# Performance work log

Measured on AMD Instinct MI355X. Metric: run time of the kernel, lower is better.

Reference implementation:

```python
import jax, jax.numpy as jnp
import numpy as np

NUM_EMBEDDINGS = 512
EMBEDDING_DIM = 128
COMMITMENT = 0.25
DECAY = 0.99
EPS = 1e-05


def setup_inputs() -> dict:
    key = jax.random.key(0)
    k1, k2 = jax.random.split(key)
    z = jax.random.normal(k1, (32, EMBEDDING_DIM, 64, 64), dtype=jnp.float32)
    embedding = jax.random.normal(k2, (EMBEDDING_DIM, NUM_EMBEDDINGS), dtype=jnp.float32)
    cluster_size = jnp.zeros((NUM_EMBEDDINGS,), dtype=jnp.float32)
    embed_avg = embedding  # buffer initialized as a clone of embedding
    return {"z": z, "embedding": embedding, "cluster_size": cluster_size, "embed_avg": embed_avg}


def reference(z, embedding, cluster_size, embed_avg):
    sg = jax.lax.stop_gradient
    D, K = embedding.shape
    B, C, H, W = z.shape
    z_perm = jnp.transpose(z, (0, 2, 3, 1))          # [B,H,W,D]
    flat_z = z_perm.reshape(-1, D)                    # [N,D]

    distances = ((flat_z ** 2).sum(1, keepdims=True)
                 - 2.0 * (flat_z @ embedding)
                 + (embedding ** 2).sum(0)[None, :])  # [N,K]
    idx = jnp.argmin(distances, axis=1)               # [N]

    # gather codes (equivalent to one-hot @ embedding.T, without materializing one-hot)
    quantized = jnp.take(embedding.T, idx, axis=0).reshape(z_perm.shape)  # [B,H,W,D]
    quantized = jnp.transpose(quantized, (0, 3, 1, 2))                    # [B,D,H,W]

    # EMA codebook update (training branch)
    enc_sum = jax.ops.segment_sum(jnp.ones_like(idx, dtype=flat_z.dtype), idx, num_segments=K)  # [K]
    embed_sum = jax.ops.segment_sum(flat_z, idx, num_segments=K).T                              # [D,K]
    new_cluster_size = cluster_size * DECAY + (1.0 - DECAY) * enc_sum
    new_embed_avg = embed_avg * DECAY + (1.0 - DECAY) * embed_sum
    n = jnp.maximum(new_cluster_size.sum(), 1e-05)
    cs = (new_cluster_size + EPS) / (n + K * EPS) * n
    new_embedding = new_embed_avg / cs[None, :]

    e_latent_loss = jnp.mean((sg(quantized) - z) ** 2)
    q_latent_loss = jnp.mean((quantized - sg(z)) ** 2)
    loss = q_latent_loss + COMMITMENT * e_latent_loss

    quantized_out = z + sg(quantized - z)             # straight-through
    encoding_indices = idx.reshape(B, H, W)
    return (quantized_out, loss, encoding_indices, new_embedding, new_cluster_size, new_embed_avg)
```

## Files before the change

### kernel.cpp

```cpp
#include <hip/hip_runtime.h>
#include <hip/hip_bf16.h>
#include <float.h>

typedef _Float16 f16;
typedef __attribute__((ext_vector_type(8))) _Float16 half8;
typedef __attribute__((ext_vector_type(4))) float floatx4;

#define DIM   128
#define HW    4096
#define NPOS  131072
#define K     512
#define ZSTRIDE_B 524288

#define Q_OFF     0
#define LOSS_OFF  16777216
#define IDX_OFF   16777217
#define NEMB_OFF  16908289
#define NCS_OFF   16973825
#define NEA_OFF   16974337

#define WS_E2    0
#define WS_ENC   512
#define WS_ESUM  1024
#define WS_EHI   1024
#define WS_ELO   33792
#define WS_LOSS  66560
#define WS_NN    66561

#define XST 136

__global__ __launch_bounds__(256) void k_prep(const float* __restrict__ emb,
                                              f16* __restrict__ ehiP,
                                              f16* __restrict__ eloP,
                                              float* __restrict__ e2) {
    int lin = blockIdx.x * 256 + threadIdx.x;
    int d = lin >> 9, k = lin & 511;
    float v = emb[lin];
    unsafeAtomicAdd(&e2[k], v * v);
    f16 h = (f16)v;
    f16 l = (f16)(v - (float)h);
    int g = k >> 4, r = k & 15;
    int dc = d >> 5, w = d & 31, quad = w >> 3, j = w & 7;
    int idx = (g * 4 + dc) * 512 + quad * 128 + r * 8 + j;
    ehiP[idx] = h;
    eloP[idx] = l;
}

__global__ __launch_bounds__(256, 2) void k_assign(const float* __restrict__ z,
                                                   const f16* __restrict__ ehiP,
                                                   const f16* __restrict__ eloP,
                                                   const float* __restrict__ e2,
                                                   float* __restrict__ out,
                                                   float* __restrict__ lossAcc) {
    __shared__ f16 xs_h[64 * XST];
    __shared__ f16 xs_l[64 * XST];
    __shared__ float wbD[256];
    __shared__ int   wbI[256];
    __shared__ int   bidx[64];
    __shared__ float wred[4];

    const int tid  = threadIdx.x;
    const int lane = tid & 63;
    const int wv   = tid >> 6;
    const int n0   = blockIdx.x * 64;
    const int b    = n0 >> 12;
    const int hw0  = n0 & 4095;
    const float* zb = z + b * ZSTRIDE_B + hw0;
    const int l15  = lane & 15;
    const int quad = lane >> 4;

    float sv0[16], sv1[16];
    #pragma unroll
    for (int it = 0; it < 16; ++it) {
        int lin = tid + it * 256;
        int i  = lin & 63;
        int dp = lin >> 6;
        sv0[it] = zb[(2 * dp) * HW + i];
        sv1[it] = zb[(2 * dp + 1) * HW + i];
    }
    #pragma unroll
    for (int it = 0; it < 16; ++it) {
        int lin = tid + it * 256;
        int i  = lin & 63;
        int dp = lin >> 6;
        float v0 = sv0[it], v1 = sv1[it];
        f16 h0 = (f16)v0; f16 l0 = (f16)(v0 - (float)h0);
        f16 h1 = (f16)v1; f16 l1 = (f16)(v1 - (float)h1);
        union { f16 h[2]; unsigned int u; } ph, pl;
        ph.h[0] = h0; ph.h[1] = h1;
        pl.h[0] = l0; pl.h[1] = l1;
        *(unsigned int*)&xs_h[i * XST + 2 * dp] = ph.u;
        *(unsigned int*)&xs_l[i * XST + 2 * dp] = pl.u;
    }
    __syncthreads();

    float bestD[4][4];
    int   bestI[4][4];
    #pragma unroll
    for (int t = 0; t < 4; ++t)
        #pragma unroll
        for (int r = 0; r < 4; ++r) { bestD[t][r] = FLT_MAX; bestI[t][r] = 0x7fffffff; }

    const half8* gh = (const half8*)ehiP;
    const half8* gl = (const half8*)eloP;

    for (int cc = 0; cc < 4; ++cc) {
        floatx4 acc[4][2];
        #pragma unroll
        for (int t = 0; t < 4; ++t)
            #pragma unroll
            for (int nt = 0; nt < 2; ++nt) acc[t][nt] = (floatx4){0.f, 0.f, 0.f, 0.f};

        for (int dc = 0; dc < 4; ++dc) {
            half8 ah[4], al[4];
            #pragma unroll
            for (int t = 0; t < 4; ++t) {
                int off = (t * 16 + l15) * XST + dc * 32 + quad * 8;
                ah[t] = *(const half8*)&xs_h[off];
                al[t] = *(const half8*)&xs_l[off];
            }
            #pragma unroll
            for (int nt = 0; nt < 2; ++nt) {
                int g  = cc * 8 + wv * 2 + nt;
                int bi = (g * 4 + dc) * 64 + lane;
                half8 bh = gh[bi];
                half8 bl = gl[bi];
                #pragma unroll
                for (int t = 0; t < 4; ++t) {
                    acc[t][nt] = __builtin_amdgcn_mfma_f32_16x16x32_f16(ah[t], bh, acc[t][nt], 0, 0, 0);
                    acc[t][nt] = __builtin_amdgcn_mfma_f32_16x16x32_f16(al[t], bh, acc[t][nt], 0, 0, 0);
                    acc[t][nt] = __builtin_amdgcn_mfma_f32_16x16x32_f16(ah[t], bl, acc[t][nt], 0, 0, 0);
                }
            }
        }
        #pragma unroll
        for (int nt = 0; nt < 2; ++nt) {
            int c = cc * 128 + wv * 32 + nt * 16 + l15;
            float ee = e2[c];
            #pragma unroll
            for (int t = 0; t < 4; ++t)
                #pragma unroll
                for (int r = 0; r < 4; ++r) {
                    float s = fmaf(-2.f, acc[t][nt][r], ee);
                    if (s < bestD[t][r]) { bestD[t][r] = s; bestI[t][r] = c; }
                }
        }
    }

    #pragma unroll
    for (int mask = 1; mask <= 8; mask <<= 1) {
        #pragma unroll
        for (int t = 0; t < 4; ++t)
            #pragma unroll
            for (int r = 0; r < 4; ++r) {
                float od = __shfl_xor(bestD[t][r], mask, 64);
                int   oi = __shfl_xor(bestI[t][r], mask, 64);
                if (od < bestD[t][r] || (od == bestD[t][r] && oi < bestI[t][r])) {
                    bestD[t][r] = od; bestI[t][r] = oi;
                }
            }
    }
    if (l15 == 0) {
        #pragma unroll
        for (int t = 0; t < 4; ++t)
            #pragma unroll
            for (int r = 0; r < 4; ++r) {
                int m = t * 16 + quad * 4 + r;
                wbD[wv * 64 + m] = bestD[t][r];
                wbI[wv * 64 + m] = bestI[t][r];
            }
    }
    __syncthreads();
    if (tid < 64) {
        float bd = wbD[tid]; int bi = wbI[tid];
        #pragma unroll
        for (int w = 1; w < 4; ++w) {
            float od = wbD[w * 64 + tid]; int oi = wbI[w * 64 + tid];
            if (od < bd || (od == bd && oi < bi)) { bd = od; bi = oi; }
        }
        bidx[tid] = bi;
        out[IDX_OFF + n0 + tid] = (float)bi;
    }
    __syncthreads();

    float* qb = out + Q_OFF + b * ZSTRIDE_B + hw0;
    float lsum = 0.f;
    #pragma unroll
    for (int it = 0; it < 4; ++it) {
        int o = wv * 4 + it;
        int c = bidx[lane];
        int g = c >> 4, r = c & 15;
        int base = (g * 4 + (o >> 2)) * 512 + (o & 3) * 128 + r * 8;
        half8 hh = *(const half8*)&ehiP[base];
        half8 ll = *(const half8*)&eloP[base];
        half8 zh = *(const half8*)&xs_h[lane * XST + o * 8];
        half8 zl = *(const half8*)&xs_l[lane * XST + o * 8];
        #pragma unroll
        for (int jj = 0; jj < 8; ++jj) {
            float q  = (float)hh[jj] + (float)ll[jj];
            float zz = (float)zh[jj] + (float)zl[jj];
            qb[(o * 8 + jj) * HW + lane] = q;
            float df = q - zz;
            lsum = fmaf(df, df, lsum);
        }
    }
    #pragma unroll
    for (int m = 32; m >= 1; m >>= 1) lsum += __shfl_xor(lsum, m, 64);
    if (lane == 0) wred[wv] = lsum;
    __syncthreads();
    if (tid == 0) unsafeAtomicAdd(lossAcc, wred[0] + wred[1] + wred[2] + wred[3]);
}

#define DC 8
__global__ __launch_bounds__(256) void k_ema2(const float* __restrict__ z,
                                              const float* __restrict__ out,
                                              float* __restrict__ enc,
                                              float* __restrict__ esum) {
    __shared__ float acc[DC][K];
    __shared__ float cnt[K];

    const int tid = threadIdx.x;
    const int half   = blockIdx.x & 1;
    const int dchunk = (blockIdx.x >> 1) & 15;
    const int b      = blockIdx.x >> 5;
    const int d0 = dchunk * DC;
    const bool doCnt = (dchunk == 0);

    for (int i = tid; i < DC * K; i += 256) ((float*)acc)[i] = 0.f;
    if (doCnt) for (int i = tid; i < K; i += 256) cnt[i] = 0.f;
    __syncthreads();

    const float* zb  = z + b * ZSTRIDE_B;
    const float* idp = out + IDX_OFF + b * HW;

    const int p0 = half * 2048;
    for (int t = p0; t < p0 + 2048; t += 1024) {
        const int p = t + 4 * tid;
        float4 iv = *(const float4*)(idp + p);
        int k0 = (int)iv.x;
        int k1 = (int)iv.y;
        int k2 = (int)iv.z;
        int k3 = (int)iv.w;
        if (doCnt) {
            atomicAdd(&cnt[k0], 1.f); atomicAdd(&cnt[k1], 1.f);
            atomicAdd(&cnt[k2], 1.f); atomicAdd(&cnt[k3], 1.f);
        }
        #pragma unroll
        for (int d = 0; d < DC; ++d) {
            float4 zv = *(const float4*)(zb + (d0 + d) * HW + p);
            atomicAdd(&acc[d][k0], zv.x);
            atomicAdd(&acc[d][k1], zv.y);
            atomicAdd(&acc[d][k2], zv.z);
            atomicAdd(&acc[d][k3], zv.w);
        }
    }
    __syncthreads();

    const int rot = (blockIdx.x & 31) << 6;
    for (int i = tid; i < DC * K; i += 256) {
        int j = (i + rot) & (DC * K - 1);
        int d = j >> 9, k = j & 511;
        unsafeAtomicAdd(&esum[(d0 + d) * K + k], acc[d][k]);
    }
    if (doCnt) for (int i = tid; i < K; i += 256) unsafeAtomicAdd(&enc[i], cnt[i]);
}

__global__ __launch_bounds__(512) void k_final(const float* __restrict__ enc,
                                               const float* __restrict__ cs_in,
                                               const float* __restrict__ lossAcc,
                                               float* __restrict__ out,
                                               float* __restrict__ nnOut) {
    __shared__ float red[512];
    int k = threadIdx.x;
    float ncs = fmaf(cs_in[k], 0.99f, 0.01f * enc[k]);
    red[k] = ncs;
    out[NCS_OFF + k] = ncs;
    __syncthreads();
    for (int s = 256; s > 0; s >>= 1) {
        if (k < s) red[k] += red[k + s];
        __syncthreads();
    }
    if (k == 0) {
        nnOut[0] = fmaxf(red[0], 1e-5f);
        out[LOSS_OFF] = lossAcc[0] * 1.25f / 16777216.0f;
    }
}

__global__ __launch_bounds__(512) void k_final2(const float* __restrict__ esum,
                                                const float* __restrict__ eavg_in,
                                                const float* __restrict__ nnIn,
                                                float* __restrict__ out) {
    int d = blockIdx.x;
    int k = threadIdx.x;
    float nn = nnIn[0];
    float ncs = out[NCS_OFF + k];
    float cs = (ncs + 1e-5f) / (nn + (float)K * 1e-5f) * nn;
    float ea = fmaf(eavg_in[d * K + k], 0.99f, 0.01f * esum[d * K + k]);
    out[NEA_OFF + d * K + k] = ea;
    out[NEMB_OFF + d * K + k] = ea / cs;
}

extern "C" void kernel_launch(void* const* d_in, const int* in_sizes, int n_in,
                              void* d_out, int out_size, void* d_ws, size_t ws_size,
                              hipStream_t stream) {
    const float* z     = (const float*)d_in[0];
    const float* emb   = (const float*)d_in[1];
    const float* cs_in = (const float*)d_in[2];
    const float* eavg  = (const float*)d_in[3];
    float* out = (float*)d_out;
    float* wsF = (float*)d_ws;

    hipMemsetAsync(wsF + WS_E2, 0, 1024 * sizeof(float), stream);
    hipMemsetAsync(wsF + WS_LOSS, 0, sizeof(float), stream);

    k_prep<<<256, 256, 0, stream>>>(emb, (f16*)(wsF + WS_EHI), (f16*)(wsF + WS_ELO),
                                    wsF + WS_E2);
    k_assign<<<NPOS / 64, 256, 0, stream>>>(z,
                                            (const f16*)(wsF + WS_EHI),
                                            (const f16*)(wsF + WS_ELO),
                                            wsF + WS_E2, out, wsF + WS_LOSS);
    hipMemsetAsync(wsF + WS_ESUM, 0, 65536 * sizeof(float), stream);
    k_ema2<<<1024, 256, 0, stream>>>(z, out, wsF + WS_ENC, wsF + WS_ESUM);
    k_final<<<1, 512, 0, stream>>>(wsF + WS_ENC, cs_in, wsF + WS_LOSS,
                                   out, wsF + WS_NN);
    k_final2<<<128, 512, 0, stream>>>(wsF + WS_ESUM, eavg, wsF + WS_NN, out);
}
```

Measured before the change: 302.8 us.

## Compute EMA segment sums with one-hot MFMA instead of LDS atomics

Rewrites the embed_sum scatter kernel to build one-hot fp16 tiles per 16-code group and accumulate z·onehot with MFMA in registers. z is split into hi/lo fp16 halves to keep near-fp32 accuracy. A per-wave bitmask skips code groups that no position uses. Each block now covers 16 dims instead of 8, halving the block count, and the four waves' partial results are reduced through shared memory. This removes heavy LDS float atomics, at the cost of many MFMAs, large register use (32 accumulators) and serialized per-wave reduction.

```diff
diff --git a/kernel.cpp b/kernel.cpp
--- a/kernel.cpp
+++ b/kernel.cpp
@@ -211,58 +211,115 @@
     if (tid == 0) unsafeAtomicAdd(lossAcc, wred[0] + wred[1] + wred[2] + wred[3]);
 }
 
-#define DC 8
 __global__ __launch_bounds__(256) void k_ema2(const float* __restrict__ z,
                                               const float* __restrict__ out,
                                               float* __restrict__ enc,
                                               float* __restrict__ esum) {
-    __shared__ float acc[DC][K];
-    __shared__ float cnt[K];
-
-    const int tid = threadIdx.x;
+    __shared__ float red[16 * K];
+    __shared__ unsigned int hist[K];
+
+    const int tid  = threadIdx.x;
+    const int lane = tid & 63;
+    const int wv   = tid >> 6;
+    const int l15  = lane & 15;
+    const int quad = lane >> 4;
     const int half   = blockIdx.x & 1;
-    const int dchunk = (blockIdx.x >> 1) & 15;
-    const int b      = blockIdx.x >> 5;
-    const int d0 = dchunk * DC;
+    const int dchunk = (blockIdx.x >> 1) & 7;
+    const int b      = blockIdx.x >> 4;
+    const int d0 = dchunk * 16;
     const bool doCnt = (dchunk == 0);
 
-    for (int i = tid; i < DC * K; i += 256) ((float*)acc)[i] = 0.f;
-    if (doCnt) for (int i = tid; i < K; i += 256) cnt[i] = 0.f;
-    __syncthreads();
-
-    const float* zb  = z + b * ZSTRIDE_B;
+    if (doCnt) { hist[tid] = 0u; hist[tid + 256] = 0u; }
+    __syncthreads();
+
     const float* idp = out + IDX_OFF + b * HW;
-
-    const int p0 = half * 2048;
-    for (int t = p0; t < p0 + 2048; t += 1024) {
-        const int p = t + 4 * tid;
-        float4 iv = *(const float4*)(idp + p);
-        int k0 = (int)iv.x;
-        int k1 = (int)iv.y;
-        int k2 = (int)iv.z;
-        int k3 = (int)iv.w;
-        if (doCnt) {
-            atomicAdd(&cnt[k0], 1.f); atomicAdd(&cnt[k1], 1.f);
-            atomicAdd(&cnt[k2], 1.f); atomicAdd(&cnt[k3], 1.f);
-        }
-        #pragma unroll
-        for (int d = 0; d < DC; ++d) {
-            float4 zv = *(const float4*)(zb + (d0 + d) * HW + p);
-            atomicAdd(&acc[d][k0], zv.x);
-            atomicAdd(&acc[d][k1], zv.y);
-            atomicAdd(&acc[d][k2], zv.z);
-            atomicAdd(&acc[d][k3], zv.w);
-        }
-    }
-    __syncthreads();
-
-    const int rot = (blockIdx.x & 31) << 6;
-    for (int i = tid; i < DC * K; i += 256) {
-        int j = (i + rot) & (DC * K - 1);
-        int d = j >> 9, k = j & 511;
-        unsafeAtomicAdd(&esum[(d0 + d) * K + k], acc[d][k]);
-    }
-    if (doCnt) for (int i = tid; i < K; i += 256) unsafeAtomicAdd(&enc[i], cnt[i]);
+    const float* zrow = z + b * ZSTRIDE_B + (d0 + l15) * HW;
+
+    floatx4 acc[32];
+    #pragma unroll
+    for (int t = 0; t < 32; ++t) acc[t] = (floatx4){0.f, 0.f, 0.f, 0.f};
+
+    const int p_base = half * 2048 + wv * 512;
+    for (int pt = 0; pt < 16; ++pt) {
+        const int p0 = p_base + pt * 32;
+        float4 iva = *(const float4*)(idp + p0 + quad * 8);
+        float4 ivb = *(const float4*)(idp + p0 + quad * 8 + 4);
+        int v0 = (int)iva.x, v1 = (int)iva.y, v2 = (int)iva.z, v3 = (int)iva.w;
+        int v4 = (int)ivb.x, v5 = (int)ivb.y, v6 = (int)ivb.z, v7 = (int)ivb.w;
+        unsigned int m = (1u << (v0 >> 4)) | (1u << (v1 >> 4)) |
+                         (1u << (v2 >> 4)) | (1u << (v3 >> 4)) |
+                         (1u << (v4 >> 4)) | (1u << (v5 >> 4)) |
+                         (1u << (v6 >> 4)) | (1u << (v7 >> 4));
+        m |= __shfl_xor(m, 16, 64);
+        m |= __shfl_xor(m, 32, 64);
+        float4 za = *(const float4*)(zrow + p0 + quad * 8);
+        float4 zb4 = *(const float4*)(zrow + p0 + quad * 8 + 4);
+        half8 ah, al;
+        {
+            float v;
+            v = za.x;  ah[0] = (f16)v; al[0] = (f16)(v - (float)ah[0]);
+            v = za.y;  ah[1] = (f16)v; al[1] = (f16)(v - (float)ah[1]);
+            v = za.z;  ah[2] = (f16)v; al[2] = (f16)(v - (float)ah[2]);
+            v = za.w;  ah[3] = (f16)v; al[3] = (f16)(v - (float)ah[3]);
+            v = zb4.x; ah[4] = (f16)v; al[4] = (f16)(v - (float)ah[4]);
+            v = zb4.y; ah[5] = (f16)v; al[5] = (f16)(v - (float)ah[5]);
+            v = zb4.z; ah[6] = (f16)v; al[6] = (f16)(v - (float)ah[6]);
+            v = zb4.w; ah[7] = (f16)v; al[7] = (f16)(v - (float)ah[7]);
+        }
+        #pragma unroll
+        for (int t = 0; t < 32; ++t) {
+            if (m & (1u << t)) {
+                const int target = t * 16 + l15;
+                half8 bh;
+                bh[0] = (v0 == target) ? (f16)1 : (f16)0;
+                bh[1] = (v1 == target) ? (f16)1 : (f16)0;
+                bh[2] = (v2 == target) ? (f16)1 : (f16)0;
+                bh[3] = (v3 == target) ? (f16)1 : (f16)0;
+                bh[4] = (v4 == target) ? (f16)1 : (f16)0;
+                bh[5] = (v5 == target) ? (f16)1 : (f16)0;
+                bh[6] = (v6 == target) ? (f16)1 : (f16)0;
+                bh[7] = (v7 == target) ? (f16)1 : (f16)0;
+                acc[t] = __builtin_amdgcn_mfma_f32_16x16x32_f16(ah, bh, acc[t], 0, 0, 0);
+                acc[t] = __builtin_amdgcn_mfma_f32_16x16x32_f16(al, bh, acc[t], 0, 0, 0);
+            }
+        }
+    }
+
+    if (doCnt) {
+        const int hp = half * 2048 + tid * 8;
+        #pragma unroll
+        for (int j = 0; j < 2; ++j) {
+            float4 iv = *(const float4*)(idp + hp + 4 * j);
+            atomicAdd(&hist[(int)iv.x], 1u);
+            atomicAdd(&hist[(int)iv.y], 1u);
+            atomicAdd(&hist[(int)iv.z], 1u);
+            atomicAdd(&hist[(int)iv.w], 1u);
+        }
+    }
+
+    #pragma unroll
+    for (int w = 0; w < 4; ++w) {
+        if (wv == w) {
+            #pragma unroll
+            for (int t = 0; t < 32; ++t)
+                #pragma unroll
+                for (int r = 0; r < 4; ++r) {
+                    int off = (quad * 4 + r) * K + t * 16 + l15;
+                    if (w == 0) red[off] = acc[t][r];
+                    else        red[off] += acc[t][r];
+                }
+        }
+        __syncthreads();
+    }
+
+    for (int i = tid; i < 16 * K; i += 256) {
+        int dd = i >> 9, k = i & 511;
+        unsafeAtomicAdd(&esum[(d0 + dd) * K + k], red[i]);
+    }
+    if (doCnt) {
+        unsafeAtomicAdd(&enc[tid], (float)hist[tid]);
+        unsafeAtomicAdd(&enc[tid + 256], (float)hist[tid + 256]);
+    }
 }
 
 __global__ __launch_bounds__(512) void k_final(const float* __restrict__ enc,
@@ -320,7 +377,7 @@
                                             (const f16*)(wsF + WS_ELO),
                                             wsF + WS_E2, out, wsF + WS_LOSS);
     hipMemsetAsync(wsF + WS_ESUM, 0, 65536 * sizeof(float), stream);
-    k_ema2<<<1024, 256, 0, stream>>>(z, out, wsF + WS_ENC, wsF + WS_ESUM);
+    k_ema2<<<512, 256, 0, stream>>>(z, out, wsF + WS_ENC, wsF + WS_ESUM);
     k_final<<<1, 512, 0, stream>>>(wsF + WS_ENC, cs_in, wsF + WS_LOSS,
                                    out, wsF + WS_NN);
     k_final2<<<128, 512, 0, stream>>>(wsF + WS_ESUM, eavg, wsF + WS_NN, out);
```

Result: no change. 304.1 us (+0.4%).
